# Performance work log

Hardware: AMD Instinct MI355X
Metric: run time of the kernel (lower is better)

Reference implementation:

```python
import jax, jax.numpy as jnp
from jax import lax
import numpy as np

B, A, C = 8, 49104, 90
IMG = 512.0            # 512 + compound_coef*128, coef=0
SCORE_THR = 0.2
IOU_THR = 0.2
K_PRE = 1000           # top candidates kept before NMS (standard TF-style padded NMS)
K_OUT = 100            # max detections per image


def setup_inputs() -> dict:
    key = jax.random.key(0)
    k1, k2, k3, k4, k5, k6 = jax.random.split(key, 6)
    cls_preds = jax.random.uniform(k1, (B, A, C), dtype=jnp.float32)
    loc_preds = 0.1 * jax.random.normal(k2, (B, A, 4), dtype=jnp.float32)
    # plausible anchors in (y1, x1, y2, x2) within the 512x512 image
    cy = jax.random.uniform(k3, (A,)) * IMG
    cx = jax.random.uniform(k4, (A,)) * IMG
    h = 16.0 + jax.random.uniform(k5, (A,)) * 112.0
    w = 16.0 + jax.random.uniform(k6, (A,)) * 112.0
    anchors = jnp.stack([cy - h / 2, cx - w / 2, cy + h / 2, cx + w / 2], axis=-1).astype(jnp.float32)
    return {"cls_preds": cls_preds, "loc_preds": loc_preds, "anchors": anchors}


def _decode_and_clip(anchors, loc_preds):
    # anchors: [A,4] (y1,x1,y2,x2); loc_preds: [B,A,4] (dy,dx,dh,dw)
    ya = (anchors[:, 0] + anchors[:, 2]) / 2
    xa = (anchors[:, 1] + anchors[:, 3]) / 2
    ha = anchors[:, 2] - anchors[:, 0]
    wa = anchors[:, 3] - anchors[:, 1]
    dy, dx, dh, dw = loc_preds[..., 0], loc_preds[..., 1], loc_preds[..., 2], loc_preds[..., 3]
    h = jnp.exp(dh) * ha
    w = jnp.exp(dw) * wa
    yc = dy * ha + ya
    xc = dx * wa + xa
    # output boxes in (xmin, ymin, xmax, ymax), clipped to image
    boxes = jnp.stack([xc - w / 2, yc - h / 2, xc + w / 2, yc + h / 2], axis=-1)
    return jnp.clip(boxes, 0.0, IMG)


def _pairwise_iou(boxes):
    # boxes: [K,4] xyxy -> [K,K]
    x1 = jnp.maximum(boxes[:, None, 0], boxes[None, :, 0])
    y1 = jnp.maximum(boxes[:, None, 1], boxes[None, :, 1])
    x2 = jnp.minimum(boxes[:, None, 2], boxes[None, :, 2])
    y2 = jnp.minimum(boxes[:, None, 3], boxes[None, :, 3])
    inter = jnp.clip(x2 - x1, 0.0) * jnp.clip(y2 - y1, 0.0)
    area = (boxes[:, 2] - boxes[:, 0]) * (boxes[:, 3] - boxes[:, 1])
    return inter / (area[:, None] + area[None, :] - inter + 1e-8)


def _nms_single(scores, classes, boxes):
    # scores: [A], classes: [A] int32, boxes: [A,4]
    masked = jnp.where(scores > SCORE_THR, scores, -1.0)
    vals, idx = lax.top_k(masked, K_PRE)          # top candidates
    b = boxes[idx]                                 # [K_PRE,4]
    cls = classes[idx]                             # [K_PRE]
    # batched_nms trick: offset boxes per class so cross-class IoU is 0
    off = b + cls[:, None].astype(b.dtype) * (IMG + 1.0)
    ious = _pairwise_iou(off)                      # [K_PRE,K_PRE]

    def body(keep, i):
        sup = jnp.any(keep & (ious[:, i] > IOU_THR))
        k = (vals[i] > SCORE_THR) & (~sup)
        return keep.at[i].set(k), None

    keep, _ = lax.scan(body, jnp.zeros((K_PRE,), bool), jnp.arange(K_PRE))
    final = jnp.where(keep, vals, -1.0)
    fvals, fidx = lax.top_k(final, K_OUT)
    det = fvals > 0.0
    out_boxes = jnp.where(det[:, None], b[fidx], jnp.array([0.0, 0.0, 1.0, 1.0], dtype=b.dtype))
    out_scores = jnp.where(det, fvals, 0.0)
    out_labels = jnp.where(det, cls[fidx], -1)
    return out_boxes, out_scores, out_labels


def reference(cls_preds, loc_preds, anchors):
    boxes = _decode_and_clip(anchors, loc_preds)   # [B,A,4]
    scores = jnp.max(cls_preds, axis=2)            # [B,A]
    classes = jnp.argmax(cls_preds, axis=2).astype(jnp.int32)
    out_boxes, out_scores, out_labels = jax.vmap(_nms_single)(scores, classes, boxes)
    return out_boxes, out_scores, out_labels
```

## Files before the change

### kernel.cpp

```cpp
#include <hip/hip_runtime.h>
#include <stdint.h>

#define B_    8
#define A_    49104
#define C_    90
#define IMG_  512.0f
#define THR_  0.2f
#define KPRE  1000
#define KOUT  100
#define NCAND 1024
#define NKEY  2048
#define NBIN  1024
#define BINBASE 0x17C99u
#define THRU    0xBE4CCCCDu
#define GANCH 64

static __device__ __forceinline__ uint32_t f2ord(float f) {
    uint32_t b = __float_as_uint(f);
    return (b & 0x80000000u) ? ~b : (b | 0x80000000u);
}
static __device__ __forceinline__ float ord2f(uint32_t u) {
    uint32_t b = (u & 0x80000000u) ? (u & 0x7FFFFFFFu) : ~u;
    return __uint_as_float(b);
}

__global__ __launch_bounds__(256)
void k_score_decode(const float* __restrict__ cls,
                    const float* __restrict__ loc,
                    const float* __restrict__ anc,
                    uint32_t* __restrict__ scores_u,
                    int* __restrict__ classes,
                    float* __restrict__ boxes) {
    __shared__ float4 s4[(GANCH * C_) / 4];
    __shared__ float r_val[GANCH];
    __shared__ int   r_cls[GANCH];

    int tid = threadIdx.x;
    int b = blockIdx.y;
    int a0 = blockIdx.x * GANCH;
    int valid = A_ - a0; if (valid > GANCH) valid = GANCH;

    const float4* src = (const float4*)(cls + (size_t)(b * A_ + a0) * C_);
    if (valid == GANCH) {
        float4 v0 = src[tid];
        float4 v1 = src[tid + 256];
        float4 v2 = src[tid + 512];
        float4 v3 = src[tid + 768];
        float4 v4 = src[tid + 1024];
        float4 v5;
        if (tid < 160) v5 = src[tid + 1280];
        s4[tid]        = v0;
        s4[tid + 256]  = v1;
        s4[tid + 512]  = v2;
        s4[tid + 768]  = v3;
        s4[tid + 1024] = v4;
        if (tid < 160) s4[tid + 1280] = v5;
    } else {
        int n4 = (valid * C_) / 4;
        for (int i = tid; i < n4; i += 256) s4[i] = src[i];
    }
    __syncthreads();

    const float* s = (const float*)s4;
    int g = tid >> 2, sub = tid & 3;
    float best = -1.0f; int bi = 0;
    if (g < valid) {
        #pragma unroll
        for (int j = sub; j < C_ + 2; j += 4) {
            if (j < C_) {
                float v = s[g * C_ + j];
                if (v > best) { best = v; bi = j; }
            }
        }
    }
    #pragma unroll
    for (int d = 1; d < 4; d <<= 1) {
        float ov = __shfl_xor(best, d);
        int   oi = __shfl_xor(bi, d);
        if (ov > best || (ov == best && oi < bi)) { best = ov; bi = oi; }
    }
    if (sub == 0 && g < valid) { r_val[g] = best; r_cls[g] = bi; }
    __syncthreads();

    if (tid < valid) {
        int a = a0 + tid;
        int gid = b * A_ + a;
        float bv = r_val[tid];
        float m = (bv > THR_) ? bv : -1.0f;
        scores_u[gid] = f2ord(m);
        classes[gid]  = r_cls[tid];

        float4 an = ((const float4*)anc)[a];
        float4 l4 = ((const float4*)loc)[gid];
        float ya = (an.x + an.z) * 0.5f;
        float xa = (an.y + an.w) * 0.5f;
        float ha = an.z - an.x;
        float wa = an.w - an.y;
        float h  = expf(l4.z) * ha;
        float w  = expf(l4.w) * wa;
        float yc = l4.x * ha + ya;
        float xc = l4.y * wa + xa;
        float4 bx;
        bx.x = fminf(fmaxf(xc - w * 0.5f, 0.0f), IMG_);
        bx.y = fminf(fmaxf(yc - h * 0.5f, 0.0f), IMG_);
        bx.z = fminf(fmaxf(xc + w * 0.5f, 0.0f), IMG_);
        bx.w = fminf(fmaxf(yc + h * 0.5f, 0.0f), IMG_);
        ((float4*)boxes)[gid] = bx;
    }
}

__global__ __launch_bounds__(1024)
void k_seltop(const uint32_t* __restrict__ scores_u,
              const int* __restrict__ classes,
              const float* __restrict__ boxes,
              float* __restrict__ cand_val,
              int* __restrict__ cand_cls,
              float* __restrict__ cand_box,
              int* __restrict__ n_valid) {
    int b = blockIdx.x;
    int t = threadIdx.x;
    __shared__ uint32_t h[NBIN];
    __shared__ uint64_t keys[NKEY];
    __shared__ uint32_t sh_coarse;
    __shared__ int      sh_rem;
    __shared__ uint32_t sh_cutoff;
    __shared__ int      sh_cnt;
    const uint32_t* su = scores_u + (size_t)b * A_;

    h[t] = 0;
    if (t == 0) sh_cnt = 0;
    __syncthreads();
    for (int a = t; a < A_; a += 1024) {
        uint32_t u = su[a];
        if (u > THRU) {
            int bin = (int)(u >> 15) - (int)BINBASE;
            bin = bin < 0 ? 0 : (bin >= NBIN ? NBIN - 1 : bin);
            atomicAdd(&h[bin], 1u);
        }
    }
    __syncthreads();
    for (int d = 1; d < NBIN; d <<= 1) {
        uint32_t add = (t + d < NBIN) ? h[t + d] : 0u;
        __syncthreads();
        h[t] += add;
        __syncthreads();
    }
    {
        uint32_t St = h[t];
        uint32_t Sn = (t + 1 < NBIN) ? h[t + 1] : 0u;
        if (St >= KPRE && Sn < KPRE) {
            sh_coarse = (BINBASE + (uint32_t)t) << 15;
            sh_rem = KPRE - (int)Sn;
        }
        if (t == 0 && h[0] < KPRE) {
            sh_rem = 0;
            sh_coarse = 0xFFFFFFFFu;
            sh_cutoff = BINBASE << 15;
        }
    }
    __syncthreads();
    uint32_t coarse = sh_coarse;
    int rem = sh_rem;

    h[t] = 0;
    __syncthreads();
    if (rem > 0) {
        for (int a = t; a < A_; a += 1024) {
            uint32_t u = su[a];
            if ((u & 0xFFFF8000u) == coarse)
                atomicAdd(&h[(u >> 5) & 0x3FF], 1u);
        }
    }
    __syncthreads();
    for (int d = 1; d < NBIN; d <<= 1) {
        uint32_t add = (t + d < NBIN) ? h[t + d] : 0u;
        __syncthreads();
        h[t] += add;
        __syncthreads();
    }
    if (rem > 0) {
        int St = (int)h[t];
        int Sn = (t + 1 < NBIN) ? (int)h[t + 1] : 0;
        if (St >= rem && Sn < rem)
            sh_cutoff = coarse | ((uint32_t)t << 5);
    }
    __syncthreads();
    uint32_t cutoff = sh_cutoff;

    for (int a = t; a < A_; a += 1024) {
        uint32_t u = su[a];
        if (u >= cutoff) {
            int p = atomicAdd(&sh_cnt, 1);
            if (p < NKEY)
                keys[p] = ((uint64_t)u << 32) | (uint32_t)(~(uint32_t)a);
        }
    }
    __syncthreads();
    int n = sh_cnt; if (n > NKEY) n = NKEY;

    uint64_t k0 = (t        < n) ? keys[t]        : 0ull;
    uint64_t k1 = (t + 1024 < n) ? keys[t + 1024] : 0ull;
    int r0 = 0, r1 = 0;
    #pragma unroll 4
    for (int j = 0; j < n; ++j) {
        uint64_t v = keys[j];
        r0 += (v > k0);
        r1 += (v > k1);
    }
    #pragma unroll
    for (int q = 0; q < 2; ++q) {
        int i = t + q * 1024;
        int r = q == 0 ? r0 : r1;
        uint64_t k = q == 0 ? k0 : k1;
        if (i < n && r < NCAND) {
            uint32_t u = (uint32_t)(k >> 32);
            int ai = (int)(~(uint32_t)k);
            int ci = b * NCAND + r;
            cand_val[ci] = ord2f(u);
            cand_cls[ci] = classes[(size_t)b * A_ + ai];
            ((float4*)cand_box)[ci] = ((const float4*)boxes)[(size_t)b * A_ + ai];
        }
    }
    int nn = n < NCAND ? n : NCAND;
    for (int i = nn + t; i < NCAND; i += 1024) {
        int ci = b * NCAND + i;
        cand_val[ci] = -1.0f;
        cand_cls[ci] = 0;
        float4 z; z.x = z.y = z.z = z.w = 0.0f;
        ((float4*)cand_box)[ci] = z;
    }
    if (t == 0) n_valid[b] = n < KPRE ? n : KPRE;
}

__global__ void k_masks(const float* __restrict__ cand_box,
                        const int* __restrict__ cand_cls,
                        unsigned short* __restrict__ M16) {
    int b = blockIdx.x;
    __shared__ float x1s[NCAND], y1s[NCAND], x2s[NCAND], y2s[NCAND], ars[NCAND];
    for (int i = threadIdx.x; i < NCAND; i += blockDim.x) {
        int ci = b * NCAND + i;
        float4 bx = ((const float4*)cand_box)[ci];
        float off = (float)cand_cls[ci] * (IMG_ + 1.0f);
        float ox1 = bx.x + off, oy1 = bx.y + off;
        float ox2 = bx.z + off, oy2 = bx.w + off;
        x1s[i] = ox1; y1s[i] = oy1; x2s[i] = ox2; y2s[i] = oy2;
        ars[i] = (ox2 - ox1) * (oy2 - oy1);
    }
    __syncthreads();

    int row0 = blockIdx.y * 63;
    for (int item = threadIdx.x; item < 63 * 64; item += blockDim.x) {
        int i = row0 + (item >> 6);
        if (i >= KPRE) continue;
        int w = item & 63;
        float xi1 = x1s[i], yi1 = y1s[i], xi2 = x2s[i], yi2 = y2s[i], ai = ars[i];
        unsigned int m = 0;
        int j0 = w * 16;
        #pragma unroll
        for (int t = 0; t < 16; ++t) {
            int j = j0 + t;
            float xx1 = fmaxf(xi1, x1s[j]);
            float yy1 = fmaxf(yi1, y1s[j]);
            float xx2 = fminf(xi2, x2s[j]);
            float yy2 = fminf(yi2, y2s[j]);
            float iw = xx2 - xx1; iw = iw > 0.0f ? iw : 0.0f;
            float ih = yy2 - yy1; ih = ih > 0.0f ? ih : 0.0f;
            float inter = iw * ih;
            float den = (ai + ars[j]) - inter + 1e-8f;
            float iou = inter / den;
            m |= (iou > THR_ ? 1u : 0u) << t;
        }
        M16[((size_t)(b * NCAND + i)) * 64 + w] = (unsigned short)m;
    }
}

__global__ void k_nms_out(const unsigned short* __restrict__ M16,
                          const float* __restrict__ cand_val,
                          const int* __restrict__ cand_cls,
                          const float* __restrict__ cand_box,
                          const int* __restrict__ n_valid,
                          float* __restrict__ out) {
    int b = blockIdx.x;
    int lane = threadIdx.x;
    int nv = n_valid[b]; if (nv > KPRE) nv = KPRE;
    const unsigned short* Mr = M16 + (size_t)b * NCAND * 64;
    __shared__ int kept[KOUT];

    uint32_t S = 0;
    int cnt = 0;
    uint32_t cur[8], nxt[8];
    #pragma unroll
    for (int t = 0; t < 8; ++t) cur[t] = Mr[(size_t)t * 64 + lane];

    for (int base = 0; base < nv && cnt < KOUT; base += 8) {
        #pragma unroll
        for (int t = 0; t < 8; ++t) {
            int r = base + 8 + t;
            nxt[t] = Mr[(size_t)(r < NCAND ? r : 0) * 64 + lane];
        }
        #pragma unroll
        for (int t = 0; t < 8; ++t) {
            int i = base + t;
            bool inb = (i < nv) && (cnt < KOUT);
            unsigned long long ball =
                __ballot(inb && (((S >> (i & 15)) & 1u) != 0u));
            int sup = (int)((ball >> (i >> 4)) & 1ull);
            if (inb && !sup) {
                S |= cur[t];
                if (lane == 0) kept[cnt] = i;
                cnt++;
            }
        }
        #pragma unroll
        for (int t = 0; t < 8; ++t) cur[t] = nxt[t];
    }
    __syncthreads();

    for (int s_ = lane; s_ < KOUT; s_ += 64) {
        float b0 = 0.0f, b1 = 0.0f, b2 = 1.0f, b3 = 1.0f, sc = 0.0f, lb = -1.0f;
        if (s_ < cnt) {
            int i = kept[s_];
            int ci = b * NCAND + i;
            float4 bx = ((const float4*)cand_box)[ci];
            b0 = bx.x; b1 = bx.y; b2 = bx.z; b3 = bx.w;
            sc = cand_val[ci];
            lb = (float)cand_cls[ci];
        }
        int ob = (b * KOUT + s_) * 4;
        out[ob + 0] = b0; out[ob + 1] = b1; out[ob + 2] = b2; out[ob + 3] = b3;
        out[B_ * KOUT * 4 + b * KOUT + s_] = sc;
        out[B_ * KOUT * 5 + b * KOUT + s_] = lb;
    }
}

extern "C" void kernel_launch(void* const* d_in, const int* in_sizes, int n_in,
                              void* d_out, int out_size, void* d_ws, size_t ws_size,
                              hipStream_t stream) {
    const float* cls = (const float*)d_in[0];
    const float* loc = (const float*)d_in[1];
    const float* anc = (const float*)d_in[2];
    float* out = (float*)d_out;

    char* ws = (char*)d_ws;
    size_t off = 0;
    auto alloc = [&](size_t bytes) -> void* {
        void* p = ws + off;
        off += (bytes + 255) & ~(size_t)255;
        return p;
    };
    uint32_t* scores_u = (uint32_t*)alloc((size_t)B_ * A_ * 4);
    int*      classes  = (int*)     alloc((size_t)B_ * A_ * 4);
    float*    boxes    = (float*)   alloc((size_t)B_ * A_ * 4 * 4);
    float*    cand_val = (float*)   alloc((size_t)B_ * NCAND * 4);
    int*      cand_cls = (int*)     alloc((size_t)B_ * NCAND * 4);
    float*    cand_box = (float*)   alloc((size_t)B_ * NCAND * 4 * 4);
    int*      n_valid  = (int*)     alloc((size_t)B_ * 4);
    unsigned short* M16 = (unsigned short*)alloc((size_t)B_ * NCAND * 64 * 2);

    dim3 gD((A_ + GANCH - 1) / GANCH, B_);
    k_score_decode<<<gD, 256, 0, stream>>>(
        cls, loc, anc, scores_u, classes, boxes);
    k_seltop<<<B_, 1024, 0, stream>>>(
        scores_u, classes, boxes, cand_val, cand_cls, cand_box, n_valid);
    k_masks<<<dim3(B_, 16), 256, 0, stream>>>(cand_box, cand_cls, M16);
    k_nms_out<<<B_, 64, 0, stream>>>(
        M16, cand_val, cand_cls, cand_box, n_valid, out);
}
```

Measured before the change: 322.1 us.

## Speculative single-pass top-K prefilter with histogram fallback; skip lower-triangle IoU words

```diff
diff --git a/kernel.cpp b/kernel.cpp
--- a/kernel.cpp
+++ b/kernel.cpp
@@ -119,84 +119,115 @@
               int* __restrict__ n_valid) {
     int b = blockIdx.x;
     int t = threadIdx.x;
+    int lane = t & 63;
+    __shared__ uint64_t keys[NKEY];
     __shared__ uint32_t h[NBIN];
-    __shared__ uint64_t keys[NKEY];
     __shared__ uint32_t sh_coarse;
     __shared__ int      sh_rem;
     __shared__ uint32_t sh_cutoff;
     __shared__ int      sh_cnt;
     const uint32_t* su = scores_u + (size_t)b * A_;
-
-    h[t] = 0;
+    const uint32_t PREF = f2ord(0.9997f);
+
     if (t == 0) sh_cnt = 0;
     __syncthreads();
-    for (int a = t; a < A_; a += 1024) {
-        uint32_t u = su[a];
-        if (u > THRU) {
-            int bin = (int)(u >> 15) - (int)BINBASE;
-            bin = bin < 0 ? 0 : (bin >= NBIN ? NBIN - 1 : bin);
-            atomicAdd(&h[bin], 1u);
-        }
-    }
-    __syncthreads();
-    for (int d = 1; d < NBIN; d <<= 1) {
-        uint32_t add = (t + d < NBIN) ? h[t + d] : 0u;
-        __syncthreads();
-        h[t] += add;
-        __syncthreads();
-    }
-    {
-        uint32_t St = h[t];
-        uint32_t Sn = (t + 1 < NBIN) ? h[t + 1] : 0u;
-        if (St >= KPRE && Sn < KPRE) {
-            sh_coarse = (BINBASE + (uint32_t)t) << 15;
-            sh_rem = KPRE - (int)Sn;
-        }
-        if (t == 0 && h[0] < KPRE) {
-            sh_rem = 0;
-            sh_coarse = 0xFFFFFFFFu;
-            sh_cutoff = BINBASE << 15;
-        }
-    }
-    __syncthreads();
-    uint32_t coarse = sh_coarse;
-    int rem = sh_rem;
-
-    h[t] = 0;
-    __syncthreads();
-    if (rem > 0) {
+
+    const uint4* su4 = (const uint4*)su;
+    for (int i = t; i < A_ / 4; i += 1024) {
+        uint4 v = su4[i];
+        #pragma unroll
+        for (int c = 0; c < 4; ++c) {
+            uint32_t u = (c == 0) ? v.x : (c == 1) ? v.y : (c == 2) ? v.z : v.w;
+            unsigned long long m = __ballot(u >= PREF);
+            if (m) {
+                uint32_t base;
+                if (lane == 0) base = atomicAdd((uint32_t*)&sh_cnt, (uint32_t)__popcll(m));
+                base = __shfl((int)base, 0);
+                if (u >= PREF) {
+                    int p = (int)base +
+                            (int)__popcll(m & ((1ull << lane) - 1ull));
+                    if (p < NKEY)
+                        keys[p] = ((uint64_t)u << 32) |
+                                  (uint32_t)(~(uint32_t)(4 * i + c));
+                }
+            }
+        }
+    }
+    __syncthreads();
+    int n = sh_cnt;
+
+    if (n < KPRE || n > NKEY) {
+        h[t] = 0;
+        if (t == 0) sh_cnt = 0;
+        __syncthreads();
         for (int a = t; a < A_; a += 1024) {
             uint32_t u = su[a];
-            if ((u & 0xFFFF8000u) == coarse)
-                atomicAdd(&h[(u >> 5) & 0x3FF], 1u);
-        }
-    }
-    __syncthreads();
-    for (int d = 1; d < NBIN; d <<= 1) {
-        uint32_t add = (t + d < NBIN) ? h[t + d] : 0u;
-        __syncthreads();
-        h[t] += add;
-        __syncthreads();
-    }
-    if (rem > 0) {
-        int St = (int)h[t];
-        int Sn = (t + 1 < NBIN) ? (int)h[t + 1] : 0;
-        if (St >= rem && Sn < rem)
-            sh_cutoff = coarse | ((uint32_t)t << 5);
-    }
-    __syncthreads();
-    uint32_t cutoff = sh_cutoff;
-
-    for (int a = t; a < A_; a += 1024) {
-        uint32_t u = su[a];
-        if (u >= cutoff) {
-            int p = atomicAdd(&sh_cnt, 1);
-            if (p < NKEY)
-                keys[p] = ((uint64_t)u << 32) | (uint32_t)(~(uint32_t)a);
-        }
-    }
-    __syncthreads();
-    int n = sh_cnt; if (n > NKEY) n = NKEY;
+            if (u > THRU) {
+                int bin = (int)(u >> 15) - (int)BINBASE;
+                bin = bin < 0 ? 0 : (bin >= NBIN ? NBIN - 1 : bin);
+                atomicAdd(&h[bin], 1u);
+            }
+        }
+        __syncthreads();
+        for (int d = 1; d < NBIN; d <<= 1) {
+            uint32_t add = (t + d < NBIN) ? h[t + d] : 0u;
+            __syncthreads();
+            h[t] += add;
+            __syncthreads();
+        }
+        {
+            uint32_t St = h[t];
+            uint32_t Sn = (t + 1 < NBIN) ? h[t + 1] : 0u;
+            if (St >= KPRE && Sn < KPRE) {
+                sh_coarse = (BINBASE + (uint32_t)t) << 15;
+                sh_rem = KPRE - (int)Sn;
+            }
+            if (t == 0 && h[0] < KPRE) {
+                sh_rem = 0;
+                sh_coarse = 0xFFFFFFFFu;
+                sh_cutoff = BINBASE << 15;
+            }
+        }
+        __syncthreads();
+        uint32_t coarse = sh_coarse;
+        int rem = sh_rem;
+
+        h[t] = 0;
+        __syncthreads();
+        if (rem > 0) {
+            for (int a = t; a < A_; a += 1024) {
+                uint32_t u = su[a];
+                if ((u & 0xFFFF8000u) == coarse)
+                    atomicAdd(&h[(u >> 5) & 0x3FF], 1u);
+            }
+        }
+        __syncthreads();
+        for (int d = 1; d < NBIN; d <<= 1) {
+            uint32_t add = (t + d < NBIN) ? h[t + d] : 0u;
+            __syncthreads();
+            h[t] += add;
+            __syncthreads();
+        }
+        if (rem > 0) {
+            int St = (int)h[t];
+            int Sn = (t + 1 < NBIN) ? (int)h[t + 1] : 0;
+            if (St >= rem && Sn < rem)
+                sh_cutoff = coarse | ((uint32_t)t << 5);
+        }
+        __syncthreads();
+        uint32_t cutoff = sh_cutoff;
+
+        for (int a = t; a < A_; a += 1024) {
+            uint32_t u = su[a];
+            if (u >= cutoff) {
+                int p = atomicAdd(&sh_cnt, 1);
+                if (p < NKEY)
+                    keys[p] = ((uint64_t)u << 32) | (uint32_t)(~(uint32_t)a);
+            }
+        }
+        __syncthreads();
+        n = sh_cnt; if (n > NKEY) n = NKEY;
+    }
 
     uint64_t k0 = (t        < n) ? keys[t]        : 0ull;
     uint64_t k1 = (t + 1024 < n) ? keys[t + 1024] : 0ull;
@@ -253,6 +284,7 @@
         int i = row0 + (item >> 6);
         if (i >= KPRE) continue;
         int w = item & 63;
+        if (w < (i >> 4)) continue;
         float xi1 = x1s[i], yi1 = y1s[i], xi2 = x2s[i], yi2 = y2s[i], ai = ars[i];
         unsigned int m = 0;
         int j0 = w * 16;
```

Result: faster. 308.7 us (-4.2%).

## Prefilter top candidates in decode kernel and fuse sort with greedy NMS

Applied to the files above, without the earlier changes.

```diff
diff --git a/kernel.cpp b/kernel.cpp
--- a/kernel.cpp
+++ b/kernel.cpp
@@ -14,6 +14,7 @@
 #define BINBASE 0x17C99u
 #define THRU    0xBE4CCCCDu
 #define GANCH 64
+#define PREF_F 0.9997f
 
 static __device__ __forceinline__ uint32_t f2ord(float f) {
     uint32_t b = __float_as_uint(f);
@@ -30,7 +31,9 @@
                     const float* __restrict__ anc,
                     uint32_t* __restrict__ scores_u,
                     int* __restrict__ classes,
-                    float* __restrict__ boxes) {
+                    float* __restrict__ boxes,
+                    uint64_t* __restrict__ keysg,
+                    uint32_t* __restrict__ pcnt) {
     __shared__ float4 s4[(GANCH * C_) / 4];
     __shared__ float r_val[GANCH];
     __shared__ int   r_cls[GANCH];
@@ -39,6 +42,13 @@
     int b = blockIdx.y;
     int a0 = blockIdx.x * GANCH;
     int valid = A_ - a0; if (valid > GANCH) valid = GANCH;
+
+    float4 an, l4;
+    if (tid < valid) {
+        int a = a0 + tid;
+        an = ((const float4*)anc)[a];
+        l4 = ((const float4*)loc)[(size_t)b * A_ + a];
+    }
 
     const float4* src = (const float4*)(cls + (size_t)(b * A_ + a0) * C_);
     if (valid == GANCH) {
@@ -82,16 +92,16 @@
     if (sub == 0 && g < valid) { r_val[g] = best; r_cls[g] = bi; }
     __syncthreads();
 
+    uint32_t u = 0;
+    int aidx = a0 + tid;
     if (tid < valid) {
-        int a = a0 + tid;
-        int gid = b * A_ + a;
+        int gid = b * A_ + aidx;
         float bv = r_val[tid];
         float m = (bv > THR_) ? bv : -1.0f;
-        scores_u[gid] = f2ord(m);
+        u = f2ord(m);
+        scores_u[gid] = u;
         classes[gid]  = r_cls[tid];
 
-        float4 an = ((const float4*)anc)[a];
-        float4 l4 = ((const float4*)loc)[gid];
         float ya = (an.x + an.z) * 0.5f;
         float xa = (an.y + an.w) * 0.5f;
         float ha = an.z - an.x;
@@ -107,96 +117,123 @@
         bx.w = fminf(fmaxf(yc + h * 0.5f, 0.0f), IMG_);
         ((float4*)boxes)[gid] = bx;
     }
+
+    const uint32_t PREF = f2ord(PREF_F);
+    bool pass = (tid < valid) && (u >= PREF);
+    unsigned long long mm = __ballot(pass);
+    if (mm) {
+        int lane = tid & 63;
+        uint32_t base;
+        if (lane == 0) base = atomicAdd(&pcnt[b], (uint32_t)__popcll(mm));
+        base = (uint32_t)__shfl((int)base, 0);
+        if (pass) {
+            int p = (int)base + (int)__popcll(mm & ((1ull << lane) - 1ull));
+            if (p < NKEY)
+                keysg[(size_t)b * NKEY + p] =
+                    ((uint64_t)u << 32) | (uint32_t)(~(uint32_t)aidx);
+        }
+    }
 }
 
 __global__ __launch_bounds__(1024)
-void k_seltop(const uint32_t* __restrict__ scores_u,
-              const int* __restrict__ classes,
-              const float* __restrict__ boxes,
-              float* __restrict__ cand_val,
-              int* __restrict__ cand_cls,
-              float* __restrict__ cand_box,
-              int* __restrict__ n_valid) {
+void k_sort_nms(const uint32_t* __restrict__ scores_u,
+                const uint32_t* __restrict__ pcnt,
+                const uint64_t* __restrict__ keysg,
+                const int* __restrict__ classes,
+                const float* __restrict__ boxes,
+                float* __restrict__ out) {
     int b = blockIdx.x;
     int t = threadIdx.x;
+    __shared__ uint64_t keys[NKEY];
     __shared__ uint32_t h[NBIN];
-    __shared__ uint64_t keys[NKEY];
+    __shared__ float4   c_box[NCAND];
+    __shared__ float    c_val[NCAND];
+    __shared__ int      c_cls[NCAND];
+    __shared__ float kx1[128], ky1[128], kx2[128], ky2[128], kar[128];
+    __shared__ int   kidx[KOUT];
     __shared__ uint32_t sh_coarse;
     __shared__ int      sh_rem;
     __shared__ uint32_t sh_cutoff;
     __shared__ int      sh_cnt;
     const uint32_t* su = scores_u + (size_t)b * A_;
 
-    h[t] = 0;
-    if (t == 0) sh_cnt = 0;
-    __syncthreads();
-    for (int a = t; a < A_; a += 1024) {
-        uint32_t u = su[a];
-        if (u > THRU) {
-            int bin = (int)(u >> 15) - (int)BINBASE;
-            bin = bin < 0 ? 0 : (bin >= NBIN ? NBIN - 1 : bin);
-            atomicAdd(&h[bin], 1u);
-        }
-    }
-    __syncthreads();
-    for (int d = 1; d < NBIN; d <<= 1) {
-        uint32_t add = (t + d < NBIN) ? h[t + d] : 0u;
-        __syncthreads();
-        h[t] += add;
-        __syncthreads();
-    }
-    {
-        uint32_t St = h[t];
-        uint32_t Sn = (t + 1 < NBIN) ? h[t + 1] : 0u;
-        if (St >= KPRE && Sn < KPRE) {
-            sh_coarse = (BINBASE + (uint32_t)t) << 15;
-            sh_rem = KPRE - (int)Sn;
-        }
-        if (t == 0 && h[0] < KPRE) {
-            sh_rem = 0;
-            sh_coarse = 0xFFFFFFFFu;
-            sh_cutoff = BINBASE << 15;
-        }
-    }
-    __syncthreads();
-    uint32_t coarse = sh_coarse;
-    int rem = sh_rem;
-
-    h[t] = 0;
-    __syncthreads();
-    if (rem > 0) {
+    int n = (int)pcnt[b];
+    if (n >= KPRE && n <= NKEY) {
+        for (int i = t; i < n; i += 1024)
+            keys[i] = keysg[(size_t)b * NKEY + i];
+        __syncthreads();
+    } else {
+        h[t] = 0;
+        if (t == 0) sh_cnt = 0;
+        __syncthreads();
         for (int a = t; a < A_; a += 1024) {
             uint32_t u = su[a];
-            if ((u & 0xFFFF8000u) == coarse)
-                atomicAdd(&h[(u >> 5) & 0x3FF], 1u);
-        }
-    }
-    __syncthreads();
-    for (int d = 1; d < NBIN; d <<= 1) {
-        uint32_t add = (t + d < NBIN) ? h[t + d] : 0u;
-        __syncthreads();
-        h[t] += add;
-        __syncthreads();
-    }
-    if (rem > 0) {
-        int St = (int)h[t];
-        int Sn = (t + 1 < NBIN) ? (int)h[t + 1] : 0;
-        if (St >= rem && Sn < rem)
-            sh_cutoff = coarse | ((uint32_t)t << 5);
-    }
-    __syncthreads();
-    uint32_t cutoff = sh_cutoff;
-
-    for (int a = t; a < A_; a += 1024) {
-        uint32_t u = su[a];
-        if (u >= cutoff) {
-            int p = atomicAdd(&sh_cnt, 1);
-            if (p < NKEY)
-                keys[p] = ((uint64_t)u << 32) | (uint32_t)(~(uint32_t)a);
-        }
-    }
-    __syncthreads();
-    int n = sh_cnt; if (n > NKEY) n = NKEY;
+            if (u > THRU) {
+                int bin = (int)(u >> 15) - (int)BINBASE;
+                bin = bin < 0 ? 0 : (bin >= NBIN ? NBIN - 1 : bin);
+                atomicAdd(&h[bin], 1u);
+            }
+        }
+        __syncthreads();
+        for (int d = 1; d < NBIN; d <<= 1) {
+            uint32_t add = (t + d < NBIN) ? h[t + d] : 0u;
+            __syncthreads();
+            h[t] += add;
+            __syncthreads();
+        }
+        {
+            uint32_t St = h[t];
+            uint32_t Sn = (t + 1 < NBIN) ? h[t + 1] : 0u;
+            if (St >= KPRE && Sn < KPRE) {
+                sh_coarse = (BINBASE + (uint32_t)t) << 15;
+                sh_rem = KPRE - (int)Sn;
+            }
+            if (t == 0 && h[0] < KPRE) {
+                sh_rem = 0;
+                sh_coarse = 0xFFFFFFFFu;
+                sh_cutoff = BINBASE << 15;
+            }
+        }
+        __syncthreads();
+        uint32_t coarse = sh_coarse;
+        int rem = sh_rem;
+
+        h[t] = 0;
+        __syncthreads();
+        if (rem > 0) {
+            for (int a = t; a < A_; a += 1024) {
+                uint32_t u = su[a];
+                if ((u & 0xFFFF8000u) == coarse)
+                    atomicAdd(&h[(u >> 5) & 0x3FF], 1u);
+            }
+        }
+        __syncthreads();
+        for (int d = 1; d < NBIN; d <<= 1) {
+            uint32_t add = (t + d < NBIN) ? h[t + d] : 0u;
+            __syncthreads();
+            h[t] += add;
+            __syncthreads();
+        }
+        if (rem > 0) {
+            int St = (int)h[t];
+            int Sn = (t + 1 < NBIN) ? (int)h[t + 1] : 0;
+            if (St >= rem && Sn < rem)
+                sh_cutoff = coarse | ((uint32_t)t << 5);
+        }
+        __syncthreads();
+        uint32_t cutoff = sh_cutoff;
+
+        for (int a = t; a < A_; a += 1024) {
+            uint32_t u = su[a];
+            if (u >= cutoff) {
+                int p = atomicAdd(&sh_cnt, 1);
+                if (p < NKEY)
+                    keys[p] = ((uint64_t)u << 32) | (uint32_t)(~(uint32_t)a);
+            }
+        }
+        __syncthreads();
+        n = sh_cnt; if (n > NKEY) n = NKEY;
+    }
 
     uint64_t k0 = (t        < n) ? keys[t]        : 0ull;
     uint64_t k1 = (t + 1024 < n) ? keys[t + 1024] : 0ull;
@@ -215,121 +252,72 @@
         if (i < n && r < NCAND) {
             uint32_t u = (uint32_t)(k >> 32);
             int ai = (int)(~(uint32_t)k);
-            int ci = b * NCAND + r;
-            cand_val[ci] = ord2f(u);
-            cand_cls[ci] = classes[(size_t)b * A_ + ai];
-            ((float4*)cand_box)[ci] = ((const float4*)boxes)[(size_t)b * A_ + ai];
+            c_val[r] = ord2f(u);
+            c_cls[r] = classes[(size_t)b * A_ + ai];
+            c_box[r] = ((const float4*)boxes)[(size_t)b * A_ + ai];
         }
     }
     int nn = n < NCAND ? n : NCAND;
     for (int i = nn + t; i < NCAND; i += 1024) {
-        int ci = b * NCAND + i;
-        cand_val[ci] = -1.0f;
-        cand_cls[ci] = 0;
+        c_val[i] = -1.0f;
+        c_cls[i] = 0;
         float4 z; z.x = z.y = z.z = z.w = 0.0f;
-        ((float4*)cand_box)[ci] = z;
-    }
-    if (t == 0) n_valid[b] = n < KPRE ? n : KPRE;
-}
-
-__global__ void k_masks(const float* __restrict__ cand_box,
-                        const int* __restrict__ cand_cls,
-                        unsigned short* __restrict__ M16) {
-    int b = blockIdx.x;
-    __shared__ float x1s[NCAND], y1s[NCAND], x2s[NCAND], y2s[NCAND], ars[NCAND];
-    for (int i = threadIdx.x; i < NCAND; i += blockDim.x) {
-        int ci = b * NCAND + i;
-        float4 bx = ((const float4*)cand_box)[ci];
-        float off = (float)cand_cls[ci] * (IMG_ + 1.0f);
-        float ox1 = bx.x + off, oy1 = bx.y + off;
-        float ox2 = bx.z + off, oy2 = bx.w + off;
-        x1s[i] = ox1; y1s[i] = oy1; x2s[i] = ox2; y2s[i] = oy2;
-        ars[i] = (ox2 - ox1) * (oy2 - oy1);
+        c_box[i] = z;
     }
     __syncthreads();
 
-    int row0 = blockIdx.y * 63;
-    for (int item = threadIdx.x; item < 63 * 64; item += blockDim.x) {
-        int i = row0 + (item >> 6);
-        if (i >= KPRE) continue;
-        int w = item & 63;
-        float xi1 = x1s[i], yi1 = y1s[i], xi2 = x2s[i], yi2 = y2s[i], ai = ars[i];
-        unsigned int m = 0;
-        int j0 = w * 16;
-        #pragma unroll
-        for (int t = 0; t < 16; ++t) {
-            int j = j0 + t;
-            float xx1 = fmaxf(xi1, x1s[j]);
-            float yy1 = fmaxf(yi1, y1s[j]);
-            float xx2 = fminf(xi2, x2s[j]);
-            float yy2 = fminf(yi2, y2s[j]);
-            float iw = xx2 - xx1; iw = iw > 0.0f ? iw : 0.0f;
-            float ih = yy2 - yy1; ih = ih > 0.0f ? ih : 0.0f;
-            float inter = iw * ih;
-            float den = (ai + ars[j]) - inter + 1e-8f;
-            float iou = inter / den;
-            m |= (iou > THR_ ? 1u : 0u) << t;
-        }
-        M16[((size_t)(b * NCAND + i)) * 64 + w] = (unsigned short)m;
-    }
-}
-
-__global__ void k_nms_out(const unsigned short* __restrict__ M16,
-                          const float* __restrict__ cand_val,
-                          const int* __restrict__ cand_cls,
-                          const float* __restrict__ cand_box,
-                          const int* __restrict__ n_valid,
-                          float* __restrict__ out) {
-    int b = blockIdx.x;
-    int lane = threadIdx.x;
-    int nv = n_valid[b]; if (nv > KPRE) nv = KPRE;
-    const unsigned short* Mr = M16 + (size_t)b * NCAND * 64;
-    __shared__ int kept[KOUT];
-
-    uint32_t S = 0;
-    int cnt = 0;
-    uint32_t cur[8], nxt[8];
-    #pragma unroll
-    for (int t = 0; t < 8; ++t) cur[t] = Mr[(size_t)t * 64 + lane];
-
-    for (int base = 0; base < nv && cnt < KOUT; base += 8) {
-        #pragma unroll
-        for (int t = 0; t < 8; ++t) {
-            int r = base + 8 + t;
-            nxt[t] = Mr[(size_t)(r < NCAND ? r : 0) * 64 + lane];
-        }
-        #pragma unroll
-        for (int t = 0; t < 8; ++t) {
-            int i = base + t;
-            bool inb = (i < nv) && (cnt < KOUT);
-            unsigned long long ball =
-                __ballot(inb && (((S >> (i & 15)) & 1u) != 0u));
-            int sup = (int)((ball >> (i >> 4)) & 1ull);
-            if (inb && !sup) {
-                S |= cur[t];
-                if (lane == 0) kept[cnt] = i;
+    if (t < 64) {
+        int l = t;
+        int nv = n < KPRE ? n : KPRE;
+        int cnt = 0;
+        for (int i = 0; i < nv && cnt < KOUT; ++i) {
+            float4 bx = c_box[i];
+            float off = (float)c_cls[i] * (IMG_ + 1.0f);
+            float ix1 = bx.x + off, iy1 = bx.y + off;
+            float ix2 = bx.z + off, iy2 = bx.w + off;
+            float iar = (ix2 - ix1) * (iy2 - iy1);
+            bool pred = false;
+            #pragma unroll
+            for (int q = 0; q < 2; ++q) {
+                int s = l + q * 64;
+                if (s < cnt) {
+                    float xx1 = fmaxf(ix1, kx1[s]);
+                    float yy1 = fmaxf(iy1, ky1[s]);
+                    float xx2 = fminf(ix2, kx2[s]);
+                    float yy2 = fminf(iy2, ky2[s]);
+                    float iw = xx2 - xx1; iw = iw > 0.0f ? iw : 0.0f;
+                    float ih = yy2 - yy1; ih = ih > 0.0f ? ih : 0.0f;
+                    float inter = iw * ih;
+                    float den = (kar[s] + iar) - inter + 1e-8f;
+                    pred |= (inter / den > THR_);
+                }
+            }
+            if (__ballot(pred) == 0ull) {
+                if (l == 0) {
+                    kx1[cnt] = ix1; ky1[cnt] = iy1;
+                    kx2[cnt] = ix2; ky2[cnt] = iy2;
+                    kar[cnt] = iar; kidx[cnt] = i;
+                }
                 cnt++;
             }
         }
-        #pragma unroll
-        for (int t = 0; t < 8; ++t) cur[t] = nxt[t];
-    }
-    __syncthreads();
-
-    for (int s_ = lane; s_ < KOUT; s_ += 64) {
-        float b0 = 0.0f, b1 = 0.0f, b2 = 1.0f, b3 = 1.0f, sc = 0.0f, lb = -1.0f;
-        if (s_ < cnt) {
-            int i = kept[s_];
-            int ci = b * NCAND + i;
-            float4 bx = ((const float4*)cand_box)[ci];
-            b0 = bx.x; b1 = bx.y; b2 = bx.z; b3 = bx.w;
-            sc = cand_val[ci];
-            lb = (float)cand_cls[ci];
-        }
-        int ob = (b * KOUT + s_) * 4;
-        out[ob + 0] = b0; out[ob + 1] = b1; out[ob + 2] = b2; out[ob + 3] = b3;
-        out[B_ * KOUT * 4 + b * KOUT + s_] = sc;
-        out[B_ * KOUT * 5 + b * KOUT + s_] = lb;
+
+        for (int s_ = l; s_ < KOUT; s_ += 64) {
+            float b0 = 0.0f, b1 = 0.0f, b2 = 1.0f, b3 = 1.0f;
+            float sc = 0.0f, lb = -1.0f;
+            if (s_ < cnt) {
+                int i = kidx[s_];
+                float4 bx = c_box[i];
+                b0 = bx.x; b1 = bx.y; b2 = bx.z; b3 = bx.w;
+                sc = c_val[i];
+                lb = (float)c_cls[i];
+            }
+            int ob = (b * KOUT + s_) * 4;
+            out[ob + 0] = b0; out[ob + 1] = b1;
+            out[ob + 2] = b2; out[ob + 3] = b3;
+            out[B_ * KOUT * 4 + b * KOUT + s_] = sc;
+            out[B_ * KOUT * 5 + b * KOUT + s_] = lb;
+        }
     }
 }
 
@@ -351,18 +339,14 @@
     uint32_t* scores_u = (uint32_t*)alloc((size_t)B_ * A_ * 4);
     int*      classes  = (int*)     alloc((size_t)B_ * A_ * 4);
     float*    boxes    = (float*)   alloc((size_t)B_ * A_ * 4 * 4);
-    float*    cand_val = (float*)   alloc((size_t)B_ * NCAND * 4);
-    int*      cand_cls = (int*)     alloc((size_t)B_ * NCAND * 4);
-    float*    cand_box = (float*)   alloc((size_t)B_ * NCAND * 4 * 4);
-    int*      n_valid  = (int*)     alloc((size_t)B_ * 4);
-    unsigned short* M16 = (unsigned short*)alloc((size_t)B_ * NCAND * 64 * 2);
+    uint64_t* keysg    = (uint64_t*)alloc((size_t)B_ * NKEY * 8);
+    uint32_t* pcnt     = (uint32_t*)alloc((size_t)B_ * 4);
+
+    hipMemsetAsync(pcnt, 0, (size_t)B_ * 4, stream);
 
     dim3 gD((A_ + GANCH - 1) / GANCH, B_);
     k_score_decode<<<gD, 256, 0, stream>>>(
-        cls, loc, anc, scores_u, classes, boxes);
-    k_seltop<<<B_, 1024, 0, stream>>>(
-        scores_u, classes, boxes, cand_val, cand_cls, cand_box, n_valid);
-    k_masks<<<dim3(B_, 16), 256, 0, stream>>>(cand_box, cand_cls, M16);
-    k_nms_out<<<B_, 64, 0, stream>>>(
-        M16, cand_val, cand_cls, cand_box, n_valid, out);
-}
+        cls, loc, anc, scores_u, classes, boxes, keysg, pcnt);
+    k_sort_nms<<<B_, 1024, 0, stream>>>(
+        scores_u, pcnt, keysg, classes, boxes, out);
+}
```

New measurement: 313.2 us. 1.03x faster.
